# Kernel tuning notes

Measured on AMD Instinct MI355X. Metric: run time of the kernel, lower is better.

Reference implementation:

```python
import jax, jax.numpy as jnp
import numpy as np

EPS = 1e-5        # BatchNorm eps (torch default)
ALPHA = 0.2       # LeakyReLU negative slope


def _gather_nbrs(x, idx):
    # x: (B,N,C), idx: (B,P,S) -> (B,P,S,C)
    B, P, S = idx.shape
    flat = jnp.take_along_axis(x, idx.reshape(B, P * S, 1), axis=1)
    return flat.reshape(B, P, S, x.shape[-1])


def _mlp_layer(x, w, b, g, bt, m, v):
    # 1x1 Conv2d == channel matmul; BN in eval mode with running stats; ReLU.
    h = x @ w.T + b
    h = (h - m) * jax.lax.rsqrt(v + EPS) * g + bt
    return jax.nn.relu(h)


def setup_inputs() -> dict:
    key = jax.random.key(0)
    ks = jax.random.split(key, 8)
    B, N, P, S, C = 16, 4096, 1024, 32, 64
    inp = {
        "xyz": jax.random.normal(ks[0], (B, 3, N), dtype=jnp.float32),
        "points": jax.random.normal(ks[1], (B, C, N), dtype=jnp.float32),
        "fps_idx": jax.random.randint(ks[2], (B, P), 0, N, dtype=jnp.int32),
        "group_idx": jax.random.randint(ks[3], (B, P, S), 0, N, dtype=jnp.int32),
    }
    chans = [(64, 67), (64, 64), (128, 64)]
    for i, (co, ci) in enumerate(chans, start=1):
        kk = jax.random.fold_in(key, 100 + i)
        inp[f"w{i}"] = jax.random.normal(kk, (co, ci), dtype=jnp.float32) * (1.0 / np.sqrt(ci))
        inp[f"b{i}"] = jnp.zeros((co,), jnp.float32)
        inp[f"g{i}"] = jnp.ones((co,), jnp.float32)
        inp[f"beta{i}"] = jnp.zeros((co,), jnp.float32)
        inp[f"m{i}"] = jnp.zeros((co,), jnp.float32)
        inp[f"v{i}"] = jnp.ones((co,), jnp.float32)
    inp["a"] = jax.random.normal(ks[4], (3 + 128, 128), dtype=jnp.float32) * 0.1
    return inp


def reference(xyz, points, fps_idx, group_idx,
              w1, b1, g1, beta1, m1, v1,
              w2, b2, g2, beta2, m2, v2,
              w3, b3, g3, beta3, m3, v3, a):
    xyz_p = jnp.transpose(xyz, (0, 2, 1))      # (B,N,3)
    pts_p = jnp.transpose(points, (0, 2, 1))   # (B,N,C)

    # sample_and_group with precomputed fps / ball-query indices
    new_xyz = jnp.take_along_axis(xyz_p, fps_idx[:, :, None], axis=1)   # (B,P,3)
    fps_feat = jnp.take_along_axis(pts_p, fps_idx[:, :, None], axis=1)  # (B,P,C)
    grouped_xyz = _gather_nbrs(xyz_p, group_idx) - new_xyz[:, :, None, :]  # relative (B,P,S,3)
    grouped_feat = _gather_nbrs(pts_p, group_idx)                           # (B,P,S,C)

    new_points = jnp.concatenate([grouped_xyz, grouped_feat], axis=-1)  # (B,P,S,3+C)
    fps_points = jnp.concatenate([new_xyz, fps_feat], axis=-1)          # (B,P,3+C)

    layers = [(w1, b1, g1, beta1, m1, v1), (w2, b2, g2, beta2, m2, v2), (w3, b3, g3, beta3, m3, v3)]
    for (w, b, g, bt, m, v) in layers:
        new_points = _mlp_layer(new_points, w, b, g, bt, m, v)
        fps_points = _mlp_layer(fps_points, w, b, g, bt, m, v)

    # GraphAttention: delta features -> leaky-relu scores -> softmax over neighbors -> pool
    delta_p = new_xyz[:, :, None, :] - grouped_xyz        # (B,P,S,3)
    delta_h = fps_points[:, :, None, :] - new_points       # (B,P,S,D)
    e = jnp.concatenate([delta_p, delta_h], axis=-1) @ a   # (B,P,S,D)
    e = jnp.where(e > 0, e, ALPHA * e)
    attn = jax.nn.softmax(e, axis=2)                       # softmax over nsample
    pooled = jnp.sum(attn * new_points, axis=2)            # (B,P,D)

    return jnp.transpose(new_xyz, (0, 2, 1)), jnp.transpose(pooled, (0, 2, 1))
```

## Files before the change

kernel.cpp:

```cpp
#include <hip/hip_runtime.h>
#include <hip/hip_bf16.h>

#define Bn 16
#define Nn 4096
#define Pn 1024
#define Sn 32
#define Cn 64
#define EPSn 1e-5f
#define ALPHAn 0.2f
#define LOG2E 1.44269504088896341f

#define W1O 0
#define W2O 4352
#define W3O 8448
#define AO  16640
#define B1O 33536
#define B2O 33600
#define B3O 33664
#define WSF 33792
__device__ __align__(16) float g_W[WSF];

#define F1F 0
#define F2F 24
#define F3F 40
#define F5F 72
#define NFRAG 152
#define WFU (NFRAG * 512)
__device__ __align__(16) unsigned short g_Wf[WFU];

__device__ __align__(16) float g_pts[Bn * Nn * 68];
__device__ __align__(16) float g_fps[Bn * Pn * 132];

typedef __attribute__((ext_vector_type(8))) short short8;
typedef __attribute__((ext_vector_type(4))) float f32x4;

__device__ __forceinline__ void split2(float v, unsigned short& hu, unsigned short& lu) {
  __hip_bfloat16 h = __float2bfloat16(v);
  float hv = __bfloat162float(h);
  __hip_bfloat16 l = __float2bfloat16(v - hv);
  hu = *(unsigned short*)&h;
  lu = *(unsigned short*)&l;
}
__device__ __forceinline__ unsigned short bfh(float v) {
  __hip_bfloat16 h = __float2bfloat16(v);
  return *(unsigned short*)&h;
}
__device__ __forceinline__ float bf2f(unsigned short u) {
  __hip_bfloat16 h = *(__hip_bfloat16*)&u;
  return __bfloat162float(h);
}

#define MFMA_BF16 __builtin_amdgcn_mfma_f32_16x16x32_bf16
#define TERM3(Ci, Ahh, All, Bh, Bl) \
    Ci = MFMA_BF16(Ahh, Bh, Ci, 0, 0, 0); \
    Ci = MFMA_BF16(Ahh, Bl, Ci, 0, 0, 0); \
    Ci = MFMA_BF16(All, Bh, Ci, 0, 0, 0);

__global__ __launch_bounds__(256) void prep_kernel(
    const float* __restrict__ xyz, const float* __restrict__ points,
    const float* __restrict__ w1, const float* __restrict__ b1,
    const float* __restrict__ g1, const float* __restrict__ bt1,
    const float* __restrict__ m1, const float* __restrict__ v1,
    const float* __restrict__ w2, const float* __restrict__ b2,
    const float* __restrict__ g2, const float* __restrict__ bt2,
    const float* __restrict__ m2, const float* __restrict__ v2,
    const float* __restrict__ w3, const float* __restrict__ b3,
    const float* __restrict__ g3, const float* __restrict__ bt3,
    const float* __restrict__ m3, const float* __restrict__ v3,
    const float* __restrict__ a)
{
  if (blockIdx.x < 1024) {
    __shared__ float T[68 * 65];
    const int t = threadIdx.x;
    const int b = blockIdx.x >> 6, n0 = (blockIdx.x & 63) << 6;
    const int nn = t & 63, cgrp = t >> 6;
    #pragma unroll
    for (int k = 0; k < 16; ++k) {
      const int c = cgrp * 16 + k;
      T[c * 65 + nn] = points[(b * Cn + c) * Nn + n0 + nn];
    }
    if (cgrp == 0) {
      #pragma unroll
      for (int d = 0; d < 3; ++d)
        T[(64 + d) * 65 + nn] = xyz[(b * 3 + d) * Nn + n0 + nn];
      T[67 * 65 + nn] = 0.f;
    }
    __syncthreads();
    const int row = t >> 2, part = t & 3;
    float* dst = g_pts + (((long)b << 12) + n0 + row) * 68 + part * 16;
    #pragma unroll
    for (int j = 0; j < 4; ++j) {
      const int o = part * 16 + j * 4;
      float4 v = { T[(o + 0) * 65 + row], T[(o + 1) * 65 + row],
                   T[(o + 2) * 65 + row], T[(o + 3) * 65 + row] };
      *(float4*)(dst + j * 4) = v;
    }
    if (part == 3) {
      float4 v = { T[64 * 65 + row], T[65 * 65 + row],
                   T[66 * 65 + row], T[67 * 65 + row] };
      *(float4*)(dst + 16) = v;
    }
    return;
  }
  const int idx = (blockIdx.x - 1024) * blockDim.x + threadIdx.x;
  if (idx < WSF) {
    float val;
    if (idx < W2O) {
      const int k = idx >> 6, o = idx & 63;
      const float sc = g1[o] * rsqrtf(v1[o] + EPSn);
      val = (k < 64) ? w1[o * 67 + 3 + k] * sc
          : (k < 67) ? w1[o * 67 + (k - 64)] * sc : 0.f;
    } else if (idx < W3O) {
      const int r = idx - W2O, k = r >> 6, o = r & 63;
      val = w2[o * 64 + k] * (g2[o] * rsqrtf(v2[o] + EPSn));
    } else if (idx < AO) {
      const int r = idx - W3O, k = r >> 7, o = r & 127;
      val = w3[o * 64 + k] * (g3[o] * rsqrtf(v3[o] + EPSn));
    } else if (idx < B1O) {
      int r = idx - AO;
      const int half = r / 8448; r -= half * 8448;
      const int k = r >> 6, o = half * 64 + (r & 63);
      val = (k < 128) ? a[(3 + k) * 128 + o]
          : (k < 131) ? a[(k - 128) * 128 + o] : 0.f;
    } else if (idx < B2O) {
      const int o = idx - B1O;
      val = (b1[o] - m1[o]) * (g1[o] * rsqrtf(v1[o] + EPSn)) + bt1[o];
    } else if (idx < B3O) {
      const int o = idx - B2O;
      val = (b2[o] - m2[o]) * (g2[o] * rsqrtf(v2[o] + EPSn)) + bt2[o];
    } else {
      const int o = idx - B3O;
      val = (b3[o] - m3[o]) * (g3[o] * rsqrtf(v3[o] + EPSn)) + bt3[o];
    }
    g_W[idx] = val;
  } else if (idx < WSF + WFU) {
    const int i = idx - WSF;
    const int frag = i >> 9, r = i & 511;
    const int lane = r >> 3, j = r & 7;
    const int quad = lane >> 4, nn = lane & 15;
    int plane, n, k;
    float w;
    if (frag < F2F) {
      const int f = frag;
      plane = f & 1;
      const int c = (f >> 1) & 1, kcch = f >> 2, kc = kcch % 3, ch = kcch / 3;
      n = ch * 32 + c * 16 + nn; k = kc * 32 + quad * 8 + j;
      const float s = g1[n] * rsqrtf(v1[n] + EPSn);
      w = (k < 64) ? w1[n * 67 + 3 + k] * s
        : (k < 67) ? w1[n * 67 + (k - 64)] * s : 0.f;
    } else if (frag < F3F) {
      const int f = frag - F2F;
      plane = f & 1;
      const int c = (f >> 1) & 1, kc = (f >> 2) & 1, ch = f >> 3;
      n = ch * 32 + c * 16 + nn; k = kc * 32 + quad * 8 + j;
      w = w2[n * 64 + k] * (g2[n] * rsqrtf(v2[n] + EPSn));
    } else if (frag < F5F) {
      const int f = frag - F3F;
      plane = f & 1;
      const int c = (f >> 1) & 3, kc = (f >> 3) & 1, ch = f >> 4;
      n = ch * 64 + c * 16 + nn; k = kc * 32 + quad * 8 + j;
      w = w3[n * 64 + k] * (g3[n] * rsqrtf(v3[n] + EPSn));
    } else {
      const int f = frag - F5F;
      plane = f & 1;
      const int c = (f >> 1) & 3, kcch = f >> 3, kc = kcch % 5, ch = kcch / 5;
      n = ch * 64 + c * 16 + nn; k = kc * 32 + quad * 8 + j;
      w = ((k < 128) ? a[(3 + k) * 128 + n]
        : (k < 131) ? a[(k - 128) * 128 + n] : 0.f) * LOG2E;
    }
    unsigned short hu, lu; split2(w, hu, lu);
    g_Wf[i] = plane ? lu : hu;
  }
}

#define XAs 88
#define XHs 152

__global__ __launch_bounds__(256) void fps_kernel(
    const int* __restrict__ fps_idx, float* __restrict__ out)
{
  __shared__ __align__(16) unsigned char LB[15376];
  unsigned short* XAh = (unsigned short*)(LB + 0);
  unsigned short* XAl = (unsigned short*)(LB + 2816);
  unsigned short* XHh = (unsigned short*)(LB + 5632);
  unsigned short* XHl = (unsigned short*)(LB + 10496);
  unsigned short* ZS  = (unsigned short*)(LB + 15360);

  const int t = threadIdx.x, lane = t & 63, w = t >> 6;
  const int quad = lane >> 4, nn = lane & 15;
  const int ch = w >> 1, cl = w & 1;
  const int blk = ((blockIdx.x & 7) << 7) | (blockIdx.x >> 3);
  const int g0 = blk * 16;

  if (t < 4) ((float*)ZS)[t] = 0.f;

  if (t < 128) {
    const int s0 = t >> 3, cg = t & 7;
    const int gp = g0 + s0, b = gp >> 10, p = gp & 1023;
    const int fi = fps_idx[gp];
    const float* frow = g_pts + (((long)b << 12) + fi) * 68;
    const int c0 = cg * 8;
    const float4 va = *(const float4*)(frow + c0);
    const float4 vb = *(const float4*)(frow + c0 + 4);
    short8 hv, lv;
    unsigned short hu, lu;
    split2(va.x, hu, lu); hv[0] = (short)hu; lv[0] = (short)lu;
    split2(va.y, hu, lu); hv[1] = (short)hu; lv[1] = (short)lu;
    split2(va.z, hu, lu); hv[2] = (short)hu; lv[2] = (short)lu;
    split2(va.w, hu, lu); hv[3] = (short)hu; lv[3] = (short)lu;
    split2(vb.x, hu, lu); hv[4] = (short)hu; lv[4] = (short)lu;
    split2(vb.y, hu, lu); hv[5] = (short)hu; lv[5] = (short)lu;
    split2(vb.z, hu, lu); hv[6] = (short)hu; lv[6] = (short)lu;
    split2(vb.w, hu, lu); hv[7] = (short)hu; lv[7] = (short)lu;
    *(short8*)(XAh + s0 * XAs + c0) = hv;
    *(short8*)(XAl + s0 * XAs + c0) = lv;
    if (cg == 0) {
      #pragma unroll
      for (int d = 0; d < 3; ++d) {
        const float v = frow[64 + d];
        unsigned short h2, l2; split2(v, h2, l2);
        XAh[s0 * XAs + 64 + d] = h2; XAl[s0 * XAs + 64 + d] = l2;
        XHh[s0 * XHs + 128 + d] = h2; XHl[s0 * XHs + 128 + d] = l2;
        out[(b * 3 + d) * Pn + p] = v;
        g_fps[(long)gp * 132 + 128 + d] = v;
      }
    } else if (cg == 1) {
      #pragma unroll
      for (int j = 0; j < 13; ++j) { XAh[s0 * XAs + 67 + j] = 0; XAl[s0 * XAs + 67 + j] = 0; }
    } else if (cg == 2) {
      #pragma unroll
      for (int j = 0; j < 13; ++j) { XHh[s0 * XHs + 131 + j] = 0; XHl[s0 * XHs + 131 + j] = 0; }
    }
  }
  __syncthreads();

  f32x4 C[2];
  const int col1 = w * 16 + nn;

  {
    const float bb = g_W[B1O + col1];
    C[0] = (f32x4){bb, bb, bb, bb};
  }
  #pragma unroll
  for (int kc = 0; kc < 3; ++kc) {
    const int ka = kc * 32 + quad * 8;
    const short8 A0h = (ka < 80) ? *(const short8*)(XAh + nn * XAs + ka) : *(const short8*)ZS;
    const short8 A0l = (ka < 80) ? *(const short8*)(XAl + nn * XAs + ka) : *(const short8*)ZS;
    const unsigned short* pf = g_Wf + (((ch * 3 + kc) * 2 + cl) * 2) * 512 + lane * 8;
    const short8 Bh = *(const short8*)pf, Bl = *(const short8*)(pf + 512);
    TERM3(C[0], A0h, A0l, Bh, Bl);
  }
  #pragma unroll
  for (int r = 0; r < 4; ++r) {
    const float v = fmaxf(C[0][r], 0.f);
    unsigned short hu, lu; split2(v, hu, lu);
    XHh[(quad * 4 + r) * XHs + col1] = hu;
    XHl[(quad * 4 + r) * XHs + col1] = lu;
  }
  __syncthreads();

  {
    const float bb = g_W[B2O + col1];
    C[0] = (f32x4){bb, bb, bb, bb};
  }
  #pragma unroll
  for (int kc = 0; kc < 2; ++kc) {
    const int ka = kc * 32 + quad * 8;
    const short8 A0h = *(const short8*)(XHh + nn * XHs + ka);
    const short8 A0l = *(const short8*)(XHl + nn * XHs + ka);
    const unsigned short* pf = g_Wf + (F2F + ((ch * 2 + kc) * 2 + cl) * 2) * 512 + lane * 8;
    const short8 Bh = *(const short8*)pf, Bl = *(const short8*)(pf + 512);
    TERM3(C[0], A0h, A0l, Bh, Bl);
  }
  __syncthreads();
  #pragma unroll
  for (int r = 0; r < 4; ++r) {
    const float v = fmaxf(C[0][r], 0.f);
    unsigned short hu, lu; split2(v, hu, lu);
    XAh[(quad * 4 + r) * XAs + col1] = hu;
    XAl[(quad * 4 + r) * XAs + col1] = lu;
  }
  __syncthreads();

  {
    const float b0 = g_W[B3O + w * 32 + nn];
    const float b1 = g_W[B3O + w * 32 + 16 + nn];
    C[0] = (f32x4){b0, b0, b0, b0};
    C[1] = (f32x4){b1, b1, b1, b1};
  }
  #pragma unroll
  for (int kc = 0; kc < 2; ++kc) {
    const int ka = kc * 32 + quad * 8;
    const short8 A0h = *(const short8*)(XAh + nn * XAs + ka);
    const short8 A0l = *(const short8*)(XAl + nn * XAs + ka);
    #pragma unroll
    for (int c2 = 0; c2 < 2; ++c2) {
      const unsigned short* pf = g_Wf + (F3F + ((ch * 2 + kc) * 4 + cl * 2 + c2) * 2) * 512 + lane * 8;
      const short8 Bh = *(const short8*)pf, Bl = *(const short8*)(pf + 512);
      TERM3(C[c2], A0h, A0l, Bh, Bl);
    }
  }
  __syncthreads();
  #pragma unroll
  for (int c2 = 0; c2 < 2; ++c2) {
    const int col = w * 32 + c2 * 16 + nn;
    #pragma unroll
    for (int r = 0; r < 4; ++r) {
      const float v = fmaxf(C[c2][r], 0.f);
      unsigned short hu, lu; split2(v, hu, lu);
      XHh[(quad * 4 + r) * XHs + col] = hu;
      XHl[(quad * 4 + r) * XHs + col] = lu;
    }
  }
  __syncthreads();

  C[0] = (f32x4){0.f,0.f,0.f,0.f}; C[1] = C[0];
  #pragma unroll
  for (int kc = 0; kc < 5; ++kc) {
    const int ka = kc * 32 + quad * 8;
    const short8 A0h = (ka < 144) ? *(const short8*)(XHh + nn * XHs + ka) : *(const short8*)ZS;
    const short8 A0l = (ka < 144) ? *(const short8*)(XHl + nn * XHs + ka) : *(const short8*)ZS;
    #pragma unroll
    for (int c2 = 0; c2 < 2; ++c2) {
      const unsigned short* pf = g_Wf + (F5F + ((ch * 5 + kc) * 4 + cl * 2 + c2) * 2) * 512 + lane * 8;
      const short8 Bh = *(const short8*)pf, Bl = *(const short8*)(pf + 512);
      TERM3(C[c2], A0h, A0l, Bh, Bl);
    }
  }
  #pragma unroll
  for (int c2 = 0; c2 < 2; ++c2) {
    const int col = w * 32 + c2 * 16 + nn;
    #pragma unroll
    for (int r = 0; r < 4; ++r)
      g_fps[(long)(g0 + quad * 4 + r) * 132 + col] = C[c2][r];
  }
}

#define OXA0 0
#define OXA1 5632
#define OXH0 11264
#define OXH1 20992
#define OFS  30720
#define OZS  31744
#define LDSB 31760

__global__ __launch_bounds__(256, 5) void fused_kernel(
    const int* __restrict__ group_idx, float* __restrict__ out)
{
  __shared__ __align__(16) unsigned char LB[LDSB];
  unsigned short* const XA0 = (unsigned short*)(LB + OXA0);
  unsigned short* const XA1 = (unsigned short*)(LB + OXA1);
  unsigned short* const XH0 = (unsigned short*)(LB + OXH0);
  unsigned short* const XH1 = (unsigned short*)(LB + OXH1);
  float*          FS = (float*)(LB + OFS);
  unsigned short* ZS = (unsigned short*)(LB + OZS);

  const int t = threadIdx.x, lane = t & 63, w = t >> 6;
  const int quad = lane >> 4, nn = lane & 15;
  const int ch = w >> 1, cl = w & 1;
  const int blk = ((blockIdx.x & 7) << 10) | (blockIdx.x >> 3);
  const int base = blk * 2;
  const int b = base >> 10, p0 = base & 1023;

  {
    const int gi = t >> 7, cc = t & 127;
    FS[t] = g_fps[(long)(base + gi) * 132 + cc];
  }
  if (t < 4) ((float*)ZS)[t] = 0.f;

  {
    const int s0 = t >> 3, cg = t & 7;
    const int c0 = cg * 8;
    #pragma unroll
    for (int gi = 0; gi < 2; ++gi) {
      unsigned short* XAg = gi ? XA1 : XA0;
      unsigned short* XHg = gi ? XH1 : XH0;
      const int gidx = group_idx[(base + gi) * Sn + s0];
      const float* prow = g_pts + (((long)b << 12) + gidx) * 68;
      const float4 va = *(const float4*)(prow + c0);
      const float4 vb = *(const float4*)(prow + c0 + 4);
      unsigned q0, q1, q2, q3;
      asm("v_cvt_pk_bf16_f32 %0, %1, %2" : "=v"(q0) : "v"(va.x), "v"(va.y));
      asm("v_cvt_pk_bf16_f32 %0, %1, %2" : "=v"(q1) : "v"(va.z), "v"(va.w));
      asm("v_cvt_pk_bf16_f32 %0, %1, %2" : "=v"(q2) : "v"(vb.x), "v"(vb.y));
      asm("v_cvt_pk_bf16_f32 %0, %1, %2" : "=v"(q3) : "v"(vb.z), "v"(vb.w));
      uint4 hv = {q0, q1, q2, q3};
      *(uint4*)(XAg + s0 * XAs + c0) = hv;
      if (cg == 0) {
        #pragma unroll
        for (int d = 0; d < 3; ++d) {
          const float r = prow[64 + d] - g_fps[(long)(base + gi) * 132 + 128 + d];
          const unsigned short hu = bfh(r);
          XAg[s0 * XAs + 64 + d] = hu;
          XHg[s0 * XHs + 128 + d] = hu;
        }
      } else if (cg == 1) {
        #pragma unroll
        for (int j = 0; j < 13; ++j) XAg[s0 * XAs + 67 + j] = 0;
      } else if (cg == 2) {
        #pragma unroll
        for (int j = 0; j < 13; ++j) XHg[s0 * XHs + 131 + j] = 0;
      }
    }
  }
  __syncthreads();

  const int col1 = w * 16 + nn;

  {
    f32x4 C00, C01, C10, C11;
    const float bb = g_W[B1O + col1];
    C00 = (f32x4){bb, bb, bb, bb};
    C01 = C00; C10 = C00; C11 = C00;
    #pragma unroll
    for (int kc = 0; kc < 3; ++kc) {
      const int ka = kc * 32 + quad * 8;
      const unsigned short* pf = g_Wf + (((ch * 3 + kc) * 2 + cl) * 2) * 512 + lane * 8;
      const short8 Bh = *(const short8*)pf, Bl = *(const short8*)(pf + 512);
      const short8 A00 = (ka < 80) ? *(const short8*)(XA0 + nn * XAs + ka) : *(const short8*)ZS;
      const short8 A01 = (ka < 80) ? *(const short8*)(XA0 + (16 + nn) * XAs + ka) : *(const short8*)ZS;
      const short8 A10 = (ka < 80) ? *(const short8*)(XA1 + nn * XAs + ka) : *(const short8*)ZS;
      const short8 A11 = (ka < 80) ? *(const short8*)(XA1 + (16 + nn) * XAs + ka) : *(const short8*)ZS;
      C00 = MFMA_BF16(A00, Bh, C00, 0, 0, 0);
      C00 = MFMA_BF16(A00, Bl, C00, 0, 0, 0);
      C01 = MFMA_BF16(A01, Bh, C01, 0, 0, 0);
      C01 = MFMA_BF16(A01, Bl, C01, 0, 0, 0);
      C10 = MFMA_BF16(A10, Bh, C10, 0, 0, 0);
      C10 = MFMA_BF16(A10, Bl, C10, 0, 0, 0);
      C11 = MFMA_BF16(A11, Bh, C11, 0, 0, 0);
      C11 = MFMA_BF16(A11, Bl, C11, 0, 0, 0);
    }
    #pragma unroll
    for (int r = 0; r < 4; ++r) {
      XH0[(quad * 4 + r) * XHs + col1]      = bfh(fmaxf(C00[r], 0.f));
      XH0[(16 + quad * 4 + r) * XHs + col1] = bfh(fmaxf(C01[r], 0.f));
      XH1[(quad * 4 + r) * XHs + col1]      = bfh(fmaxf(C10[r], 0.f));
      XH1[(16 + quad * 4 + r) * XHs + col1] = bfh(fmaxf(C11[r], 0.f));
    }
  }
  __syncthreads();

  {
    f32x4 C00, C01, C10, C11;
    const float bb = g_W[B2O + col1];
    C00 = (f32x4){bb, bb, bb, bb};
    C01 = C00; C10 = C00; C11 = C00;
    #pragma unroll
    for (int kc = 0; kc < 2; ++kc) {
      const int ka = kc * 32 + quad * 8;
      const unsigned short* pf = g_Wf + (F2F + ((ch * 2 + kc) * 2 + cl) * 2) * 512 + lane * 8;
      const short8 Bh = *(const short8*)pf, Bl = *(const short8*)(pf + 512);
      const short8 A00 = *(const short8*)(XH0 + nn * XHs + ka);
      const short8 A01 = *(const short8*)(XH0 + (16 + nn) * XHs + ka);
      const short8 A10 = *(const short8*)(XH1 + nn * XHs + ka);
      const short8 A11 = *(const short8*)(XH1 + (16 + nn) * XHs + ka);
      C00 = MFMA_BF16(A00, Bh, C00, 0, 0, 0);
      C00 = MFMA_BF16(A00, Bl, C00, 0, 0, 0);
      C01 = MFMA_BF16(A01, Bh, C01, 0, 0, 0);
      C01 = MFMA_BF16(A01, Bl, C01, 0, 0, 0);
      C10 = MFMA_BF16(A10, Bh, C10, 0, 0, 0);
      C10 = MFMA_BF16(A10, Bl, C10, 0, 0, 0);
      C11 = MFMA_BF16(A11, Bh, C11, 0, 0, 0);
      C11 = MFMA_BF16(A11, Bl, C11, 0, 0, 0);
    }
    #pragma unroll
    for (int r = 0; r < 4; ++r) {
      XA0[(quad * 4 + r) * XAs + col1]      = bfh(fmaxf(C00[r], 0.f));
      XA0[(16 + quad * 4 + r) * XAs + col1] = bfh(fmaxf(C01[r], 0.f));
      XA1[(quad * 4 + r) * XAs + col1]      = bfh(fmaxf(C10[r], 0.f));
      XA1[(16 + quad * 4 + r) * XAs + col1] = bfh(fmaxf(C11[r], 0.f));
    }
  }
  __syncthreads();

  {
    f32x4 C0[4], C1[4];
    const float b0 = g_W[B3O + w * 32 + nn];
    const float b1 = g_W[B3O + w * 32 + 16 + nn];
    C0[0] = (f32x4){b0, b0, b0, b0};
    C0[1] = (f32x4){b1, b1, b1, b1};
    C0[2] = C0[0]; C0[3] = C0[1];
    C1[0] = C0[0]; C1[1] = C0[1]; C1[2] = C0[0]; C1[3] = C0[1];
    #pragma unroll
    for (int kc = 0; kc < 2; ++kc) {
      const int ka = kc * 32 + quad * 8;
      const short8 A00 = *(const short8*)(XA0 + nn * XAs + ka);
      const short8 A01 = *(const short8*)(XA0 + (16 + nn) * XAs + ka);
      const short8 A10 = *(const short8*)(XA1 + nn * XAs + ka);
      const short8 A11 = *(const short8*)(XA1 + (16 + nn) * XAs + ka);
      #pragma unroll
      for (int c2 = 0; c2 < 2; ++c2) {
        const unsigned short* pf = g_Wf + (F3F + ((ch * 2 + kc) * 4 + cl * 2 + c2) * 2) * 512 + lane * 8;
        const short8 Bh = *(const short8*)pf, Bl = *(const short8*)(pf + 512);
        C0[0 + c2] = MFMA_BF16(A00, Bh, C0[0 + c2], 0, 0, 0);
        C0[0 + c2] = MFMA_BF16(A00, Bl, C0[0 + c2], 0, 0, 0);
        C0[2 + c2] = MFMA_BF16(A01, Bh, C0[2 + c2], 0, 0, 0);
        C0[2 + c2] = MFMA_BF16(A01, Bl, C0[2 + c2], 0, 0, 0);
        C1[0 + c2] = MFMA_BF16(A10, Bh, C1[0 + c2], 0, 0, 0);
        C1[0 + c2] = MFMA_BF16(A10, Bl, C1[0 + c2], 0, 0, 0);
        C1[2 + c2] = MFMA_BF16(A11, Bh, C1[2 + c2], 0, 0, 0);
        C1[2 + c2] = MFMA_BF16(A11, Bl, C1[2 + c2], 0, 0, 0);
      }
    }
    #pragma unroll
    for (int c2 = 0; c2 < 2; ++c2) {
      const int col = w * 32 + c2 * 16 + nn;
      #pragma unroll
      for (int r = 0; r < 4; ++r) {
        XH0[(quad * 4 + r) * XHs + col]      = bfh(fmaxf(C0[0 + c2][r], 0.f));
        XH0[(16 + quad * 4 + r) * XHs + col] = bfh(fmaxf(C0[2 + c2][r], 0.f));
        XH1[(quad * 4 + r) * XHs + col]      = bfh(fmaxf(C1[0 + c2][r], 0.f));
        XH1[(16 + quad * 4 + r) * XHs + col] = bfh(fmaxf(C1[2 + c2][r], 0.f));
      }
    }
  }
  __syncthreads();

  f32x4 C0[4], C1[4];
  {
    const float e00 = FS[w * 32 + nn];
    const float e01 = FS[w * 32 + 16 + nn];
    const float e10 = FS[128 + w * 32 + nn];
    const float e11 = FS[128 + w * 32 + 16 + nn];
    C0[0] = (f32x4){-e00, -e00, -e00, -e00};
    C0[1] = (f32x4){-e01, -e01, -e01, -e01};
    C0[2] = C0[0]; C0[3] = C0[1];
    C1[0] = (f32x4){-e10, -e10, -e10, -e10};
    C1[1] = (f32x4){-e11, -e11, -e11, -e11};
    C1[2] = C1[0]; C1[3] = C1[1];
  }
  #pragma unroll
  for (int kc = 0; kc < 5; ++kc) {
    const int ka = kc * 32 + quad * 8;
    const short8 A00 = (ka < 144) ? *(const short8*)(XH0 + nn * XHs + ka) : *(const short8*)ZS;
    const short8 A01 = (ka < 144) ? *(const short8*)(XH0 + (16 + nn) * XHs + ka) : *(const short8*)ZS;
    const short8 A10 = (ka < 144) ? *(const short8*)(XH1 + nn * XHs + ka) : *(const short8*)ZS;
    const short8 A11 = (ka < 144) ? *(const short8*)(XH1 + (16 + nn) * XHs + ka) : *(const short8*)ZS;
    #pragma unroll
    for (int c2 = 0; c2 < 2; ++c2) {
      const unsigned short* pf = g_Wf + (F5F + ((ch * 5 + kc) * 4 + cl * 2 + c2) * 2) * 512 + lane * 8;
      const short8 Bh = *(const short8*)pf, Bl = *(const short8*)(pf + 512);
      C0[0 + c2] = MFMA_BF16(A00, Bh, C0[0 + c2], 0, 0, 0);
      C0[0 + c2] = MFMA_BF16(A00, Bl, C0[0 + c2], 0, 0, 0);
      C0[2 + c2] = MFMA_BF16(A01, Bh, C0[2 + c2], 0, 0, 0);
      C0[2 + c2] = MFMA_BF16(A01, Bl, C0[2 + c2], 0, 0, 0);
      C1[0 + c2] = MFMA_BF16(A10, Bh, C1[0 + c2], 0, 0, 0);
      C1[0 + c2] = MFMA_BF16(A10, Bl, C1[0 + c2], 0, 0, 0);
      C1[2 + c2] = MFMA_BF16(A11, Bh, C1[2 + c2], 0, 0, 0);
      C1[2 + c2] = MFMA_BF16(A11, Bl, C1[2 + c2], 0, 0, 0);
    }
  }

  #pragma unroll
  for (int gi = 0; gi < 2; ++gi) {
    unsigned short* XHg = gi ? XH1 : XH0;
    #pragma unroll
    for (int c2 = 0; c2 < 2; ++c2) {
      const int col = w * 32 + c2 * 16 + nn;
      f32x4* Cg = gi ? C1 : C0;
      float tmin = 3.4e38f;
      #pragma unroll
      for (int mi = 0; mi < 2; ++mi)
        #pragma unroll
        for (int r = 0; r < 4; ++r) {
          const int idx = mi * 2 + c2;
          const float cv = Cg[idx][r];
          const float tv = fminf(cv, 0.2f * cv);
          Cg[idx][r] = tv;
          tmin = fminf(tmin, tv);
        }
      tmin = fminf(tmin, __shfl_xor(tmin, 16));
      tmin = fminf(tmin, __shfl_xor(tmin, 32));
      float den = 0.f, pool = 0.f;
      #pragma unroll
      for (int mi = 0; mi < 2; ++mi)
        #pragma unroll
        for (int r = 0; r < 4; ++r) {
          const int idx = mi * 2 + c2;
          const float wgt = __builtin_amdgcn_exp2f(tmin - Cg[idx][r]);
          den += wgt;
          pool = fmaf(wgt, bf2f(XHg[(mi * 16 + quad * 4 + r) * XHs + col]), pool);
        }
      den  += __shfl_xor(den, 16);  den  += __shfl_xor(den, 32);
      pool += __shfl_xor(pool, 16); pool += __shfl_xor(pool, 32);
      if (quad == 0)
        out[Bn * 3 * Pn + ((b << 7) + col) * Pn + p0 + gi] =
            pool * __builtin_amdgcn_rcpf(den);
    }
  }
}

extern "C" void kernel_launch(void* const* d_in, const int* in_sizes, int n_in,
                              void* d_out, int out_size, void* d_ws, size_t ws_size,
                              hipStream_t stream) {
  const float* xyz       = (const float*)d_in[0];
  const float* points    = (const float*)d_in[1];
  const int*   fps_idx   = (const int*)d_in[2];
  const int*   group_idx = (const int*)d_in[3];

  const int prep_blocks = 1024 + (WSF + WFU + 255) / 256;
  prep_kernel<<<prep_blocks, 256, 0, stream>>>(
      xyz, points,
      (const float*)d_in[4],  (const float*)d_in[5],
      (const float*)d_in[6],  (const float*)d_in[7],
      (const float*)d_in[8],  (const float*)d_in[9],
      (const float*)d_in[10], (const float*)d_in[11],
      (const float*)d_in[12], (const float*)d_in[13],
      (const float*)d_in[14], (const float*)d_in[15],
      (const float*)d_in[16], (const float*)d_in[17],
      (const float*)d_in[18], (const float*)d_in[19],
      (const float*)d_in[20], (const float*)d_in[21],
      (const float*)d_in[22]);

  fps_kernel<<<1024, 256, 0, stream>>>(fps_idx, (float*)d_out);

  fused_kernel<<<Bn * Pn / 2, 256, 0, stream>>>(group_idx, (float*)d_out);
}
```

Baseline: 221.5 us.

## Alias activation LDS buffers into a single per-group buffer to raise occupancy

Replaces the separate XA/XH shared-memory buffers with one XB buffer per group, reusing column ranges across layers (layer-2 output goes to columns 64+). Extra barriers are inserted before in-place overwrites so reads finish before writes. This cuts LDS per block from about 31 KB to 20 KB and raises launch bounds from 5 to 7 blocks per CU, trading a couple of added syncs for higher occupancy to hide gather latency.

Result: slower. 230.9 us (+4.3%).

```diff
diff --git a/kernel.cpp b/kernel.cpp
--- a/kernel.cpp
+++ b/kernel.cpp
@@ -336,22 +336,18 @@
   }
 }
 
-#define OXA0 0
-#define OXA1 5632
-#define OXH0 11264
-#define OXH1 20992
-#define OFS  30720
-#define OZS  31744
-#define LDSB 31760
-
-__global__ __launch_bounds__(256, 5) void fused_kernel(
+#define OXB0 0
+#define OXB1 9728
+#define OFS  19456
+#define OZS  20480
+#define LDSB 20496
+
+__global__ __launch_bounds__(256, 7) void fused_kernel(
     const int* __restrict__ group_idx, float* __restrict__ out)
 {
   __shared__ __align__(16) unsigned char LB[LDSB];
-  unsigned short* const XA0 = (unsigned short*)(LB + OXA0);
-  unsigned short* const XA1 = (unsigned short*)(LB + OXA1);
-  unsigned short* const XH0 = (unsigned short*)(LB + OXH0);
-  unsigned short* const XH1 = (unsigned short*)(LB + OXH1);
+  unsigned short* const XB0 = (unsigned short*)(LB + OXB0);
+  unsigned short* const XB1 = (unsigned short*)(LB + OXB1);
   float*          FS = (float*)(LB + OFS);
   unsigned short* ZS = (unsigned short*)(LB + OZS);
 
@@ -373,8 +369,7 @@
     const int c0 = cg * 8;
     #pragma unroll
     for (int gi = 0; gi < 2; ++gi) {
-      unsigned short* XAg = gi ? XA1 : XA0;
-      unsigned short* XHg = gi ? XH1 : XH0;
+      unsigned short* XBg = gi ? XB1 : XB0;
       const int gidx = group_idx[(base + gi) * Sn + s0];
       const float* prow = g_pts + (((long)b << 12) + gidx) * 68;
       const float4 va = *(const float4*)(prow + c0);
@@ -385,21 +380,24 @@
       asm("v_cvt_pk_bf16_f32 %0, %1, %2" : "=v"(q2) : "v"(vb.x), "v"(vb.y));
       asm("v_cvt_pk_bf16_f32 %0, %1, %2" : "=v"(q3) : "v"(vb.z), "v"(vb.w));
       uint4 hv = {q0, q1, q2, q3};
-      *(uint4*)(XAg + s0 * XAs + c0) = hv;
+      *(uint4*)(XBg + s0 * XHs + c0) = hv;
       if (cg == 0) {
         #pragma unroll
         for (int d = 0; d < 3; ++d) {
           const float r = prow[64 + d] - g_fps[(long)(base + gi) * 132 + 128 + d];
           const unsigned short hu = bfh(r);
-          XAg[s0 * XAs + 64 + d] = hu;
-          XHg[s0 * XHs + 128 + d] = hu;
+          XBg[s0 * XHs + 64 + d] = hu;
+          XBg[s0 * XHs + 128 + d] = hu;
         }
       } else if (cg == 1) {
         #pragma unroll
-        for (int j = 0; j < 13; ++j) XAg[s0 * XAs + 67 + j] = 0;
+        for (int j = 0; j < 15; ++j) XBg[s0 * XHs + 67 + j] = 0;
       } else if (cg == 2) {
         #pragma unroll
-        for (int j = 0; j < 13; ++j) XHg[s0 * XHs + 131 + j] = 0;
+        for (int j = 0; j < 14; ++j) XBg[s0 * XHs + 82 + j] = 0;
+      } else if (cg == 3) {
+        #pragma unroll
+        for (int j = 0; j < 13; ++j) XBg[s0 * XHs + 131 + j] = 0;
       }
     }
   }
@@ -417,10 +415,10 @@
       const int ka = kc * 32 + quad * 8;
       const unsigned short* pf = g_Wf + (((ch * 3 + kc) * 2 + cl) * 2) * 512 + lane * 8;
       const short8 Bh = *(const short8*)pf, Bl = *(const short8*)(pf + 512);
-      const short8 A00 = (ka < 80) ? *(const short8*)(XA0 + nn * XAs + ka) : *(const short8*)ZS;
-      const short8 A01 = (ka < 80) ? *(const short8*)(XA0 + (16 + nn) * XAs + ka) : *(const short8*)ZS;
-      const short8 A10 = (ka < 80) ? *(const short8*)(XA1 + nn * XAs + ka) : *(const short8*)ZS;
-      const short8 A11 = (ka < 80) ? *(const short8*)(XA1 + (16 + nn) * XAs + ka) : *(const short8*)ZS;
+      const short8 A00 = *(const short8*)(XB0 + nn * XHs + ka);
+      const short8 A01 = *(const short8*)(XB0 + (16 + nn) * XHs + ka);
+      const short8 A10 = *(const short8*)(XB1 + nn * XHs + ka);
+      const short8 A11 = *(const short8*)(XB1 + (16 + nn) * XHs + ka);
       C00 = MFMA_BF16(A00, Bh, C00, 0, 0, 0);
       C00 = MFMA_BF16(A00, Bl, C00, 0, 0, 0);
       C01 = MFMA_BF16(A01, Bh, C01, 0, 0, 0);
@@ -430,12 +428,13 @@
       C11 = MFMA_BF16(A11, Bh, C11, 0, 0, 0);
       C11 = MFMA_BF16(A11, Bl, C11, 0, 0, 0);
     }
+    __syncthreads();
     #pragma unroll
     for (int r = 0; r < 4; ++r) {
-      XH0[(quad * 4 + r) * XHs + col1]      = bfh(fmaxf(C00[r], 0.f));
-      XH0[(16 + quad * 4 + r) * XHs + col1] = bfh(fmaxf(C01[r], 0.f));
-      XH1[(quad * 4 + r) * XHs + col1]      = bfh(fmaxf(C10[r], 0.f));
-      XH1[(16 + quad * 4 + r) * XHs + col1] = bfh(fmaxf(C11[r], 0.f));
+      XB0[(quad * 4 + r) * XHs + col1]      = bfh(fmaxf(C00[r], 0.f));
+      XB0[(16 + quad * 4 + r) * XHs + col1] = bfh(fmaxf(C01[r], 0.f));
+      XB1[(quad * 4 + r) * XHs + col1]      = bfh(fmaxf(C10[r], 0.f));
+      XB1[(16 + quad * 4 + r) * XHs + col1] = bfh(fmaxf(C11[r], 0.f));
     }
   }
   __syncthreads();
@@ -450,10 +449,10 @@
       const int ka = kc * 32 + quad * 8;
       const unsigned short* pf = g_Wf + (F2F + ((ch * 2 + kc) * 2 + cl) * 2) * 512 + lane * 8;
       const short8 Bh = *(const short8*)pf, Bl = *(const short8*)(pf + 512);
-      const short8 A00 = *(const short8*)(XH0 + nn * XHs + ka);
-      const short8 A01 = *(const short8*)(XH0 + (16 + nn) * XHs + ka);
-      const short8 A10 = *(const short8*)(XH1 + nn * XHs + ka);
-      const short8 A11 = *(const short8*)(XH1 + (16 + nn) * XHs + ka);
+      const short8 A00 = *(const short8*)(XB0 + nn * XHs + ka);
+      const short8 A01 = *(const short8*)(XB0 + (16 + nn) * XHs + ka);
+      const short8 A10 = *(const short8*)(XB1 + nn * XHs + ka);
+      const short8 A11 = *(const short8*)(XB1 + (16 + nn) * XHs + ka);
       C00 = MFMA_BF16(A00, Bh, C00, 0, 0, 0);
       C00 = MFMA_BF16(A00, Bl, C00, 0, 0, 0);
       C01 = MFMA_BF16(A01, Bh, C01, 0, 0, 0);
@@ -465,10 +464,10 @@
     }
     #pragma unroll
     for (int r = 0; r < 4; ++r) {
-      XA0[(quad * 4 + r) * XAs + col1]      = bfh(fmaxf(C00[r], 0.f));
-      XA0[(16 + quad * 4 + r) * XAs + col1] = bfh(fmaxf(C01[r], 0.f));
-      XA1[(quad * 4 + r) * XAs + col1]      = bfh(fmaxf(C10[r], 0.f));
-      XA1[(16 + quad * 4 + r) * XAs + col1] = bfh(fmaxf(C11[r], 0.f));
+      XB0[(quad * 4 + r) * XHs + 64 + col1]      = bfh(fmaxf(C00[r], 0.f));
+      XB0[(16 + quad * 4 + r) * XHs + 64 + col1] = bfh(fmaxf(C01[r], 0.f));
+      XB1[(quad * 4 + r) * XHs + 64 + col1]      = bfh(fmaxf(C10[r], 0.f));
+      XB1[(16 + quad * 4 + r) * XHs + 64 + col1] = bfh(fmaxf(C11[r], 0.f));
     }
   }
   __syncthreads();
@@ -483,11 +482,11 @@
     C1[0] = C0[0]; C1[1] = C0[1]; C1[2] = C0[0]; C1[3] = C0[1];
     #pragma unroll
     for (int kc = 0; kc < 2; ++kc) {
-      const int ka = kc * 32 + quad * 8;
-      const short8 A00 = *(const short8*)(XA0 + nn * XAs + ka);
-      const short8 A01 = *(const short8*)(XA0 + (16 + nn) * XAs + ka);
-      const short8 A10 = *(const short8*)(XA1 + nn * XAs + ka);
-      const short8 A11 = *(const short8*)(XA1 + (16 + nn) * XAs + ka);
+      const int ka = 64 + kc * 32 + quad * 8;
+      const short8 A00 = *(const short8*)(XB0 + nn * XHs + ka);
+      const short8 A01 = *(const short8*)(XB0 + (16 + nn) * XHs + ka);
+      const short8 A10 = *(const short8*)(XB1 + nn * XHs + ka);
+      const short8 A11 = *(const short8*)(XB1 + (16 + nn) * XHs + ka);
       #pragma unroll
       for (int c2 = 0; c2 < 2; ++c2) {
         const unsigned short* pf = g_Wf + (F3F + ((ch * 2 + kc) * 4 + cl * 2 + c2) * 2) * 512 + lane * 8;
@@ -502,15 +501,16 @@
         C1[2 + c2] = MFMA_BF16(A11, Bl, C1[2 + c2], 0, 0, 0);
       }
     }
+    __syncthreads();
     #pragma unroll
     for (int c2 = 0; c2 < 2; ++c2) {
       const int col = w * 32 + c2 * 16 + nn;
       #pragma unroll
       for (int r = 0; r < 4; ++r) {
-        XH0[(quad * 4 + r) * XHs + col]      = bfh(fmaxf(C0[0 + c2][r], 0.f));
-        XH0[(16 + quad * 4 + r) * XHs + col] = bfh(fmaxf(C0[2 + c2][r], 0.f));
-        XH1[(quad * 4 + r) * XHs + col]      = bfh(fmaxf(C1[0 + c2][r], 0.f));
-        XH1[(16 + quad * 4 + r) * XHs + col] = bfh(fmaxf(C1[2 + c2][r], 0.f));
+        XB0[(quad * 4 + r) * XHs + col]      = bfh(fmaxf(C0[0 + c2][r], 0.f));
+        XB0[(16 + quad * 4 + r) * XHs + col] = bfh(fmaxf(C0[2 + c2][r], 0.f));
+        XB1[(quad * 4 + r) * XHs + col]      = bfh(fmaxf(C1[0 + c2][r], 0.f));
+        XB1[(16 + quad * 4 + r) * XHs + col] = bfh(fmaxf(C1[2 + c2][r], 0.f));
       }
     }
   }
@@ -532,10 +532,10 @@
   #pragma unroll
   for (int kc = 0; kc < 5; ++kc) {
     const int ka = kc * 32 + quad * 8;
-    const short8 A00 = (ka < 144) ? *(const short8*)(XH0 + nn * XHs + ka) : *(const short8*)ZS;
-    const short8 A01 = (ka < 144) ? *(const short8*)(XH0 + (16 + nn) * XHs + ka) : *(const short8*)ZS;
-    const short8 A10 = (ka < 144) ? *(const short8*)(XH1 + nn * XHs + ka) : *(const short8*)ZS;
-    const short8 A11 = (ka < 144) ? *(const short8*)(XH1 + (16 + nn) * XHs + ka) : *(const short8*)ZS;
+    const short8 A00 = (ka < 144) ? *(const short8*)(XB0 + nn * XHs + ka) : *(const short8*)ZS;
+    const short8 A01 = (ka < 144) ? *(const short8*)(XB0 + (16 + nn) * XHs + ka) : *(const short8*)ZS;
+    const short8 A10 = (ka < 144) ? *(const short8*)(XB1 + nn * XHs + ka) : *(const short8*)ZS;
+    const short8 A11 = (ka < 144) ? *(const short8*)(XB1 + (16 + nn) * XHs + ka) : *(const short8*)ZS;
     #pragma unroll
     for (int c2 = 0; c2 < 2; ++c2) {
       const unsigned short* pf = g_Wf + (F5F + ((ch * 5 + kc) * 4 + cl * 2 + c2) * 2) * 512 + lane * 8;
@@ -553,7 +553,7 @@
 
   #pragma unroll
   for (int gi = 0; gi < 2; ++gi) {
-    unsigned short* XHg = gi ? XH1 : XH0;
+    unsigned short* XBg = gi ? XB1 : XB0;
     #pragma unroll
     for (int c2 = 0; c2 < 2; ++c2) {
       const int col = w * 32 + c2 * 16 + nn;
@@ -579,7 +579,7 @@
           const int idx = mi * 2 + c2;
           const float wgt = __builtin_amdgcn_exp2f(tmin - Cg[idx][r]);
           den += wgt;
-          pool = fmaf(wgt, bf2f(XHg[(mi * 16 + quad * 4 + r) * XHs + col]), pool);
+          pool = fmaf(wgt, bf2f(XBg[(mi * 16 + quad * 4 + r) * XHs + col]), pool);
         }
       den  += __shfl_xor(den, 16);  den  += __shfl_xor(den, 32);
       pool += __shfl_xor(pool, 16); pool += __shfl_xor(pool, 32);
```
